# Performance work log

Measured on AMD Instinct MI355X. Metric: run time of the kernel, lower is better.

The kernel has to match this reference:

```python
import jax, jax.numpy as jnp
import numpy as np

N_HEADS, D_MODEL, D_HEAD = 16, 1024, 64
BATCH, SEQ = 2, 2048
INIT_RANGE = 0.02


def setup_inputs() -> dict:
    key = jax.random.key(0)
    ks = jax.random.split(key, 5)
    x = jax.random.normal(ks[0], (BATCH, SEQ, D_MODEL), dtype=jnp.float32)
    W_Q = jax.random.normal(ks[1], (N_HEADS, D_MODEL, D_HEAD), dtype=jnp.float32) * INIT_RANGE
    W_K = jax.random.normal(ks[2], (N_HEADS, D_MODEL, D_HEAD), dtype=jnp.float32) * INIT_RANGE
    W_V = jax.random.normal(ks[3], (N_HEADS, D_MODEL, D_HEAD), dtype=jnp.float32) * INIT_RANGE
    W_O = jax.random.normal(ks[4], (N_HEADS, D_HEAD, D_MODEL), dtype=jnp.float32) * INIT_RANGE
    b_Q = jnp.zeros((N_HEADS, D_HEAD), dtype=jnp.float32)
    b_K = jnp.zeros((N_HEADS, D_HEAD), dtype=jnp.float32)
    b_V = jnp.zeros((N_HEADS, D_HEAD), dtype=jnp.float32)
    b_O = jnp.zeros((D_MODEL,), dtype=jnp.float32)
    return {"normalized_resid_pre": x, "W_Q": W_Q, "W_K": W_K, "W_V": W_V,
            "W_O": W_O, "b_Q": b_Q, "b_K": b_K, "b_V": b_V, "b_O": b_O}


def reference(normalized_resid_pre, W_Q, W_K, W_V, W_O, b_Q, b_K, b_V, b_O):
    x = normalized_resid_pre  # [b, s, d_model]
    q = jnp.einsum('bsm,hmd->bshd', x, W_Q) + b_Q  # [b, s, h, d_head]
    k = jnp.einsum('bsm,hmd->bshd', x, W_K) + b_K
    v = jnp.einsum('bsm,hmd->bshd', x, W_V) + b_V
    scores = jnp.einsum('bqhd,bkhd->bhqk', q, k) / jnp.sqrt(jnp.float32(D_HEAD))
    seq = x.shape[1]
    causal = jnp.tril(jnp.ones((seq, seq), dtype=bool))  # True where allowed
    scores = jnp.where(causal, scores, jnp.float32(-jnp.inf))
    pattern = jax.nn.softmax(scores, axis=-1)  # [b, h, q, k]
    z = jnp.einsum('bhqk,bkhd->bqhd', pattern, v)
    attn_out = jnp.einsum('bqhd,hdm->bqm', z, W_O) + b_O
    return attn_out
```

## Files before the change

### kernel.cpp

```cpp
#include <hip/hip_runtime.h>
#include <hip/hip_bf16.h>

#define BATCH 2
#define SEQL 2048
#define NH 16
#define DH 64
#define DM 1024
#define LDK 72
#define QSCALE 0.1803368801111244f

typedef __hip_bfloat16 bf16;
typedef __attribute__((ext_vector_type(8))) short  bf16x8;
typedef __attribute__((ext_vector_type(4))) float  f32x4;

__device__ __forceinline__ void gl_lds16(const void* g, void* l) {
    __builtin_amdgcn_global_load_lds(
        (const __attribute__((address_space(1))) unsigned int*)g,
        (__attribute__((address_space(3))) unsigned int*)l, 16, 0, 0);
}

__global__ __launch_bounds__(256) void xconv_kernel(
    const float* __restrict__ x, bf16* __restrict__ xb)
{
    const size_t i = ((size_t)blockIdx.x * 256 + threadIdx.x) * 4;
    const float4 v = *(const float4*)(x + i);
    bf16 o[4];
    o[0] = __float2bfloat16(v.x); o[1] = __float2bfloat16(v.y);
    o[2] = __float2bfloat16(v.z); o[3] = __float2bfloat16(v.w);
    *(uint2*)(xb + i) = *(const uint2*)o;
}

__global__ __launch_bounds__(256) void wtrans_kernel(
    const float* __restrict__ Wq, const float* __restrict__ Wk,
    const float* __restrict__ Wv, const float* __restrict__ Wo,
    bf16* __restrict__ Wt)
{
    __shared__ float ts[64][65];
    const int zi = blockIdx.z;
    const float* src = (zi == 0) ? Wq : (zi == 1) ? Wk : (zi == 2) ? Wv : Wo;
    bf16* dst = Wt + (size_t)zi * DM * DM;
    const int row0 = blockIdx.y * 64;
    const int col0 = blockIdx.x * 64;
    const int tx = threadIdx.x & 63;
    const int ty = threadIdx.x >> 6;

    if (zi < 3) {
        const int h = col0 >> 6;
        #pragma unroll
        for (int i = 0; i < 16; ++i) {
            const int r = ty + 4 * i;
            ts[r][tx] = src[h * (DM * DH) + (row0 + r) * DH + tx];
        }
    } else {
        #pragma unroll
        for (int i = 0; i < 16; ++i) {
            const int r = ty + 4 * i;
            ts[r][tx] = src[(size_t)(row0 + r) * DM + col0 + tx];
        }
    }
    __syncthreads();
    #pragma unroll
    for (int i = 0; i < 16; ++i) {
        const int rr = ty + 4 * i;
        dst[(size_t)(col0 + rr) * DM + row0 + tx] = __float2bfloat16(ts[tx][rr]);
    }
}

__global__ __launch_bounds__(256) void qkv_gemm(
    const bf16* __restrict__ xb, const bf16* __restrict__ Wt,
    const float* __restrict__ bq, const float* __restrict__ bk, const float* __restrict__ bv,
    bf16* __restrict__ qkv)
{
    __shared__ __align__(16) bf16 As[2][128 * 32];
    __shared__ __align__(16) bf16 Bs[2][128 * 32];

    const int t = threadIdx.x;
    const int lane = t & 63, w = t >> 6;
    const int ml = lane & 15, quad = lane >> 4;
    const int wr = w >> 1, wc = w & 1;
    const int bn = blockIdx.x, bm = blockIdx.y, which = blockIdx.z;

    const bf16* A0 = xb + (size_t)(bm * 128) * DM;
    const bf16* B0 = Wt + (size_t)which * DM * DM + (size_t)(bn * 128) * DM;
    const float* bias = (which == 0) ? bq : (which == 1) ? bk : bv;
    bf16* outb = qkv + (size_t)which * (BATCH * SEQL * NH * DH);
    const float oscale = (which == 0) ? QSCALE : 1.0f;

    f32x4 acc[4][4];
    #pragma unroll
    for (int i = 0; i < 4; ++i)
        #pragma unroll
        for (int j = 0; j < 4; ++j) acc[i][j] = (f32x4){0.f, 0.f, 0.f, 0.f};

    const int r0 = t >> 2, c0 = (t & 3) * 8;
    const int f1 = t + 256;
    const int r1 = f1 >> 2, c1 = (f1 & 3) * 8;

    for (int kt = 0; kt < DM / 64; ++kt) {
        const int k0 = kt * 64;
        __syncthreads();
        #pragma unroll
        for (int half = 0; half < 2; ++half) {
            const int kh = k0 + half * 32;
            gl_lds16(A0 + (size_t)r0 * DM + kh + c0, &As[half][t * 8]);
            gl_lds16(A0 + (size_t)r1 * DM + kh + c1, &As[half][f1 * 8]);
            gl_lds16(B0 + (size_t)r0 * DM + kh + c0, &Bs[half][t * 8]);
            gl_lds16(B0 + (size_t)r1 * DM + kh + c1, &Bs[half][f1 * 8]);
        }
        __syncthreads();
        #pragma unroll
        for (int half = 0; half < 2; ++half) {
            bf16x8 af[4], bfr[4];
            #pragma unroll
            for (int i = 0; i < 4; ++i)
                af[i] = *(const bf16x8*)&As[half][(wr * 64 + i * 16 + ml) * 32 + quad * 8];
            #pragma unroll
            for (int j = 0; j < 4; ++j)
                bfr[j] = *(const bf16x8*)&Bs[half][(wc * 64 + j * 16 + ml) * 32 + quad * 8];
            #pragma unroll
            for (int i = 0; i < 4; ++i)
                #pragma unroll
                for (int j = 0; j < 4; ++j)
                    acc[i][j] = __builtin_amdgcn_mfma_f32_16x16x32_bf16(af[i], bfr[j], acc[i][j], 0, 0, 0);
        }
    }

    float bb[4];
    #pragma unroll
    for (int j = 0; j < 4; ++j) bb[j] = bias[bn * 128 + wc * 64 + j * 16 + ml];

    if (which == 2) {
        #pragma unroll
        for (int i = 0; i < 4; ++i) {
            const int row0v = bm * 128 + wr * 64 + i * 16 + quad * 4;
            const int b = row0v >> 11;
            const int s0 = row0v & (SEQL - 1);
            #pragma unroll
            for (int j = 0; j < 4; ++j) {
                const int col = bn * 128 + wc * 64 + j * 16 + ml;
                const int h = col >> 6, d = col & 63;
                bf16 tmp[4];
                #pragma unroll
                for (int rg = 0; rg < 4; ++rg)
                    tmp[rg] = __float2bfloat16(acc[i][j][rg] + bb[j]);
                *(uint2*)&outb[(((size_t)(b * NH + h)) * DH + d) * SEQL + s0] =
                    *(const uint2*)tmp;
            }
        }
    } else {
        #pragma unroll
        for (int i = 0; i < 4; ++i) {
            #pragma unroll
            for (int rg = 0; rg < 4; ++rg) {
                const int row = bm * 128 + wr * 64 + i * 16 + quad * 4 + rg;
                const int b = row >> 11;
                const int s = row & (SEQL - 1);
                #pragma unroll
                for (int j = 0; j < 4; ++j) {
                    const int col = bn * 128 + wc * 64 + j * 16 + ml;
                    const int h = col >> 6, d = col & 63;
                    outb[(((size_t)(b * NH + h)) * SEQL + s) * DH + d] =
                        __float2bfloat16((acc[i][j][rg] + bb[j]) * oscale);
                }
            }
        }
    }
}

__global__ __launch_bounds__(256) void oproj_gemm(
    const bf16* __restrict__ zb, const bf16* __restrict__ Bt,
    const float* __restrict__ bo, float* __restrict__ out)
{
    __shared__ __align__(16) bf16 As[2][128 * 32];
    __shared__ __align__(16) bf16 Bs[2][64 * 32];

    const int t = threadIdx.x;
    const int lane = t & 63, w = t >> 6;
    const int ml = lane & 15, quad = lane >> 4;
    const int wr = w >> 1, wc = w & 1;
    const int bn = blockIdx.x, bm = blockIdx.y;

    const bf16* A0 = zb + (size_t)(bm * 128) * DM;
    const bf16* B0 = Bt + (size_t)(bn * 64) * DM;

    f32x4 acc[4][2];
    #pragma unroll
    for (int i = 0; i < 4; ++i)
        #pragma unroll
        for (int j = 0; j < 2; ++j) acc[i][j] = (f32x4){0.f, 0.f, 0.f, 0.f};

    const int r0 = t >> 2, c0 = (t & 3) * 8;
    const int f1 = t + 256;
    const int r1 = f1 >> 2, c1 = (f1 & 3) * 8;

    for (int kt = 0; kt < DM / 64; ++kt) {
        const int k0 = kt * 64;
        __syncthreads();
        #pragma unroll
        for (int half = 0; half < 2; ++half) {
            const int kh = k0 + half * 32;
            gl_lds16(A0 + (size_t)r0 * DM + kh + c0, &As[half][t * 8]);
            gl_lds16(A0 + (size_t)r1 * DM + kh + c1, &As[half][f1 * 8]);
            gl_lds16(B0 + (size_t)r0 * DM + kh + c0, &Bs[half][t * 8]);
        }
        __syncthreads();
        #pragma unroll
        for (int half = 0; half < 2; ++half) {
            bf16x8 af[4], bfr[2];
            #pragma unroll
            for (int i = 0; i < 4; ++i)
                af[i] = *(const bf16x8*)&As[half][(wr * 64 + i * 16 + ml) * 32 + quad * 8];
            #pragma unroll
            for (int j = 0; j < 2; ++j)
                bfr[j] = *(const bf16x8*)&Bs[half][(wc * 32 + j * 16 + ml) * 32 + quad * 8];
            #pragma unroll
            for (int i = 0; i < 4; ++i)
                #pragma unroll
                for (int j = 0; j < 2; ++j)
                    acc[i][j] = __builtin_amdgcn_mfma_f32_16x16x32_bf16(af[i], bfr[j], acc[i][j], 0, 0, 0);
        }
    }

    float bb[2];
    #pragma unroll
    for (int j = 0; j < 2; ++j) bb[j] = bo[bn * 64 + wc * 32 + j * 16 + ml];

    #pragma unroll
    for (int i = 0; i < 4; ++i) {
        #pragma unroll
        for (int rg = 0; rg < 4; ++rg) {
            const int row = bm * 128 + wr * 64 + i * 16 + quad * 4 + rg;
            #pragma unroll
            for (int j = 0; j < 2; ++j) {
                const int col = bn * 64 + wc * 32 + j * 16 + ml;
                out[(size_t)row * DM + col] = acc[i][j][rg] + bb[j];
            }
        }
    }
}

__global__ __launch_bounds__(256) void attn_kernel(
    const bf16* __restrict__ qg, const bf16* __restrict__ kg, const bf16* __restrict__ vtg,
    bf16* __restrict__ z)
{
    __shared__ bf16 KsS[64 * LDK];
    __shared__ bf16 VtS[64 * LDK];
    __shared__ bf16 PsS[4][16 * LDK];

    const int t    = threadIdx.x;
    const int lane = t & 63;
    const int w    = t >> 6;
    const int m    = lane & 15;
    const int quad = lane >> 4;

    const int bh = blockIdx.x;
    const int b  = bh >> 4;
    const int h  = bh & 15;
    const int qt = (gridDim.y - 1) - blockIdx.y;
    const int q0 = qt * 64;

    const size_t base   = (size_t)bh * SEQL * DH;
    const size_t vtbase = (size_t)bh * DH * SEQL;

    const int rp = t >> 3;
    const int d0 = (t & 7) * 8;

    bf16x8 aq[2];
    {
        const bf16* qp = qg + base + (size_t)(q0 + w * 16 + m) * DH + quad * 8;
        aq[0] = *(const bf16x8*)(qp);
        aq[1] = *(const bf16x8*)(qp + 32);
    }

    const short ob = (m == 0) ? (short)0x3F80 : (short)0;
    const bf16x8 bones = {ob, ob, ob, ob, ob, ob, ob, ob};

    f32x4 zacc[4];
    #pragma unroll
    for (int nt = 0; nt < 4; ++nt) zacc[nt] = (f32x4){0.f, 0.f, 0.f, 0.f};
    f32x4 lacc = (f32x4){0.f, 0.f, 0.f, 0.f};

    bf16* Psw = PsS[w];

    for (int kt = 0; kt <= qt; ++kt) {
        __syncthreads();
        {
            const bf16* kr = kg + base + (size_t)(kt * 64 + 2 * rp) * DH + d0;
            const bf16* vr = vtg + vtbase + (size_t)(2 * rp) * SEQL + kt * 64 + d0;
            const uint4 k0 = *(const uint4*)(kr);
            const uint4 k1 = *(const uint4*)(kr + DH);
            const uint4 v0 = *(const uint4*)(vr);
            const uint4 v1 = *(const uint4*)(vr + SEQL);
            *(uint4*)(&KsS[(2 * rp) * LDK + d0])     = k0;
            *(uint4*)(&KsS[(2 * rp + 1) * LDK + d0]) = k1;
            *(uint4*)(&VtS[(2 * rp) * LDK + d0])     = v0;
            *(uint4*)(&VtS[(2 * rp + 1) * LDK + d0]) = v1;
        }
        __syncthreads();

        f32x4 sc[4];
        #pragma unroll
        for (int nt = 0; nt < 4; ++nt) sc[nt] = (f32x4){0.f, 0.f, 0.f, 0.f};
        #pragma unroll
        for (int ks = 0; ks < 2; ++ks) {
            #pragma unroll
            for (int nt = 0; nt < 4; ++nt) {
                const bf16x8 bk = *(const bf16x8*)(&KsS[(nt * 16 + m) * LDK + ks * 32 + quad * 8]);
                sc[nt] = __builtin_amdgcn_mfma_f32_16x16x32_bf16(aq[ks], bk, sc[nt], 0, 0, 0);
            }
        }
        if (kt == qt) {
            #pragma unroll
            for (int nt = 0; nt < 4; ++nt) {
                const int col = nt * 16 + m;
                #pragma unroll
                for (int rg = 0; rg < 4; ++rg) {
                    const int row = w * 16 + quad * 4 + rg;
                    if (col > row) sc[nt][rg] = -1e30f;
                }
            }
        }

        #pragma unroll
        for (int nt = 0; nt < 4; ++nt)
            #pragma unroll
            for (int rg = 0; rg < 4; ++rg)
                Psw[(quad * 4 + rg) * LDK + nt * 16 + m] =
                    __float2bfloat16(__builtin_exp2f(sc[nt][rg]));

        #pragma unroll
        for (int ks = 0; ks < 2; ++ks) {
            const bf16x8 ap = *(const bf16x8*)(&Psw[m * LDK + ks * 32 + quad * 8]);
            lacc = __builtin_amdgcn_mfma_f32_16x16x32_bf16(ap, bones, lacc, 0, 0, 0);
            #pragma unroll
            for (int nt = 0; nt < 4; ++nt) {
                const bf16x8 bv = *(const bf16x8*)(&VtS[(nt * 16 + m) * LDK + ks * 32 + quad * 8]);
                zacc[nt] = __builtin_amdgcn_mfma_f32_16x16x32_bf16(ap, bv, zacc[nt], 0, 0, 0);
            }
        }
    }

    float invl[4];
    #pragma unroll
    for (int rg = 0; rg < 4; ++rg)
        invl[rg] = 1.f / __shfl(lacc[rg], quad * 16);
    #pragma unroll
    for (int nt = 0; nt < 4; ++nt) {
        const int d = nt * 16 + m;
        #pragma unroll
        for (int rg = 0; rg < 4; ++rg) {
            const int qrow = q0 + w * 16 + quad * 4 + rg;
            z[(((size_t)b * SEQL + qrow) * NH + h) * DH + d] =
                __float2bfloat16(zacc[nt][rg] * invl[rg]);
        }
    }
}

extern "C" void kernel_launch(void* const* d_in, const int* in_sizes, int n_in,
                              void* d_out, int out_size, void* d_ws, size_t ws_size,
                              hipStream_t stream)
{
    const float* x  = (const float*)d_in[0];
    const float* Wq = (const float*)d_in[1];
    const float* Wk = (const float*)d_in[2];
    const float* Wv = (const float*)d_in[3];
    const float* Wo = (const float*)d_in[4];
    const float* bq = (const float*)d_in[5];
    const float* bk = (const float*)d_in[6];
    const float* bv = (const float*)d_in[7];
    const float* bo = (const float*)d_in[8];
    float* out = (float*)d_out;

    const size_t TOK = (size_t)BATCH * SEQL;
    const size_t QKV = TOK * DM;
    bf16* xb  = (bf16*)d_ws;
    bf16* Wt  = xb + QKV;
    bf16* qkv = Wt + 4 * (size_t)DM * DM;
    bf16* zb  = qkv + 3 * QKV;

    xconv_kernel<<<dim3(TOK * DM / 1024), 256, 0, stream>>>(x, xb);
    wtrans_kernel<<<dim3(16, 16, 4), 256, 0, stream>>>(Wq, Wk, Wv, Wo, Wt);
    qkv_gemm<<<dim3(8, 32, 3), 256, 0, stream>>>(xb, Wt, bq, bk, bv, qkv);
    attn_kernel<<<dim3(BATCH * NH, SEQL / 64), 256, 0, stream>>>(
        qkv, qkv + QKV, qkv + 2 * QKV, zb);
    oproj_gemm<<<dim3(16, 32), 256, 0, stream>>>(zb, Wt + 3 * (size_t)DM * DM, bo, out);
}
```

Measured before the change: 192.0 us.

## Merge prep kernels and load attention K/V tiles directly into swizzled LDS

The x-conversion and weight-transpose kernels are merged into one launch, with an extra z-slice of blocks doing the x cast in a grid-strided loop, which removes one kernel launch. In the attention kernel, K and V^T tiles now go from global memory straight into LDS via global_load_lds. The padded LDK layout is replaced by an unpadded 64-wide layout with an XOR column swizzle to avoid bank conflicts. This cuts register staging and VGPR traffic, but the loads are still synchronous with compute, and the fused prep blocks with zi==4 each do 16 iterations, which may be unbalanced.

New measurement: 189.2 us. About the same (-1.5%).

```diff
diff --git a/kernel.cpp b/kernel.cpp
--- a/kernel.cpp
+++ b/kernel.cpp
@@ -19,24 +19,29 @@
         (__attribute__((address_space(3))) unsigned int*)l, 16, 0, 0);
 }
 
-__global__ __launch_bounds__(256) void xconv_kernel(
-    const float* __restrict__ x, bf16* __restrict__ xb)
-{
-    const size_t i = ((size_t)blockIdx.x * 256 + threadIdx.x) * 4;
-    const float4 v = *(const float4*)(x + i);
-    bf16 o[4];
-    o[0] = __float2bfloat16(v.x); o[1] = __float2bfloat16(v.y);
-    o[2] = __float2bfloat16(v.z); o[3] = __float2bfloat16(v.w);
-    *(uint2*)(xb + i) = *(const uint2*)o;
-}
-
-__global__ __launch_bounds__(256) void wtrans_kernel(
+__global__ __launch_bounds__(256) void prep_kernel(
+    const float* __restrict__ x,
     const float* __restrict__ Wq, const float* __restrict__ Wk,
     const float* __restrict__ Wv, const float* __restrict__ Wo,
-    bf16* __restrict__ Wt)
-{
+    bf16* __restrict__ Wt, bf16* __restrict__ xb)
+{
+    const int zi = blockIdx.z;
+    if (zi == 4) {
+        const int bid = blockIdx.y * 16 + blockIdx.x;
+        const size_t base = ((size_t)bid * 256 + threadIdx.x) * 4;
+        #pragma unroll
+        for (int it = 0; it < 16; ++it) {
+            const size_t i = base + (size_t)it * 262144;
+            const float4 v = *(const float4*)(x + i);
+            bf16 o[4];
+            o[0] = __float2bfloat16(v.x); o[1] = __float2bfloat16(v.y);
+            o[2] = __float2bfloat16(v.z); o[3] = __float2bfloat16(v.w);
+            *(uint2*)(xb + i) = *(const uint2*)o;
+        }
+        return;
+    }
+
     __shared__ float ts[64][65];
-    const int zi = blockIdx.z;
     const float* src = (zi == 0) ? Wq : (zi == 1) ? Wk : (zi == 2) ? Wv : Wo;
     bf16* dst = Wt + (size_t)zi * DM * DM;
     const int row0 = blockIdx.y * 64;
@@ -243,8 +248,8 @@
     const bf16* __restrict__ qg, const bf16* __restrict__ kg, const bf16* __restrict__ vtg,
     bf16* __restrict__ z)
 {
-    __shared__ bf16 KsS[64 * LDK];
-    __shared__ bf16 VtS[64 * LDK];
+    __shared__ __align__(16) bf16 KsS[64 * 64];
+    __shared__ __align__(16) bf16 VtS[64 * 64];
     __shared__ bf16 PsS[4][16 * LDK];
 
     const int t    = threadIdx.x;
@@ -262,8 +267,10 @@
     const size_t base   = (size_t)bh * SEQL * DH;
     const size_t vtbase = (size_t)bh * DH * SEQL;
 
-    const int rp = t >> 3;
-    const int d0 = (t & 7) * 8;
+    const int s0 = w * 128 + lane;
+    const int s1 = s0 + 64;
+    const int r0s = s0 >> 3, c0s = (s0 & 7) ^ (r0s & 7);
+    const int r1s = s1 >> 3, c1s = (s1 & 7) ^ (r1s & 7);
 
     bf16x8 aq[2];
     {
@@ -285,16 +292,11 @@
     for (int kt = 0; kt <= qt; ++kt) {
         __syncthreads();
         {
-            const bf16* kr = kg + base + (size_t)(kt * 64 + 2 * rp) * DH + d0;
-            const bf16* vr = vtg + vtbase + (size_t)(2 * rp) * SEQL + kt * 64 + d0;
-            const uint4 k0 = *(const uint4*)(kr);
-            const uint4 k1 = *(const uint4*)(kr + DH);
-            const uint4 v0 = *(const uint4*)(vr);
-            const uint4 v1 = *(const uint4*)(vr + SEQL);
-            *(uint4*)(&KsS[(2 * rp) * LDK + d0])     = k0;
-            *(uint4*)(&KsS[(2 * rp + 1) * LDK + d0]) = k1;
-            *(uint4*)(&VtS[(2 * rp) * LDK + d0])     = v0;
-            *(uint4*)(&VtS[(2 * rp + 1) * LDK + d0]) = v1;
+            const int kc = kt * 64;
+            gl_lds16(kg + base + (size_t)(kc + r0s) * DH + c0s * 8, &KsS[s0 * 8]);
+            gl_lds16(kg + base + (size_t)(kc + r1s) * DH + c1s * 8, &KsS[s1 * 8]);
+            gl_lds16(vtg + vtbase + (size_t)r0s * SEQL + kc + c0s * 8, &VtS[s0 * 8]);
+            gl_lds16(vtg + vtbase + (size_t)r1s * SEQL + kc + c1s * 8, &VtS[s1 * 8]);
         }
         __syncthreads();
 
@@ -305,7 +307,9 @@
         for (int ks = 0; ks < 2; ++ks) {
             #pragma unroll
             for (int nt = 0; nt < 4; ++nt) {
-                const bf16x8 bk = *(const bf16x8*)(&KsS[(nt * 16 + m) * LDK + ks * 32 + quad * 8]);
+                const int row = nt * 16 + m;
+                const int pc  = ((ks << 2) + quad) ^ (m & 7);
+                const bf16x8 bk = *(const bf16x8*)(&KsS[row * 64 + pc * 8]);
                 sc[nt] = __builtin_amdgcn_mfma_f32_16x16x32_bf16(aq[ks], bk, sc[nt], 0, 0, 0);
             }
         }
@@ -334,7 +338,9 @@
             lacc = __builtin_amdgcn_mfma_f32_16x16x32_bf16(ap, bones, lacc, 0, 0, 0);
             #pragma unroll
             for (int nt = 0; nt < 4; ++nt) {
-                const bf16x8 bv = *(const bf16x8*)(&VtS[(nt * 16 + m) * LDK + ks * 32 + quad * 8]);
+                const int row = nt * 16 + m;
+                const int pc  = ((ks << 2) + quad) ^ (m & 7);
+                const bf16x8 bv = *(const bf16x8*)(&VtS[row * 64 + pc * 8]);
                 zacc[nt] = __builtin_amdgcn_mfma_f32_16x16x32_bf16(ap, bv, zacc[nt], 0, 0, 0);
             }
         }
@@ -378,8 +384,7 @@
     bf16* qkv = Wt + 4 * (size_t)DM * DM;
     bf16* zb  = qkv + 3 * QKV;
 
-    xconv_kernel<<<dim3(TOK * DM / 1024), 256, 0, stream>>>(x, xb);
-    wtrans_kernel<<<dim3(16, 16, 4), 256, 0, stream>>>(Wq, Wk, Wv, Wo, Wt);
+    prep_kernel<<<dim3(16, 16, 5), 256, 0, stream>>>(x, Wq, Wk, Wv, Wo, Wt, xb);
     qkv_gemm<<<dim3(8, 32, 3), 256, 0, stream>>>(xb, Wt, bq, bk, bv, qkv);
     attn_kernel<<<dim3(BATCH * NH, SEQL / 64), 256, 0, stream>>>(
         qkv, qkv + QKV, qkv + 2 * QKV, zb);
```
